# Kernel tuning notes

Measured on AMD Instinct MI355X. Metric: run time of the kernel, lower is better.

## Reference

```python
import jax, jax.numpy as jnp
import numpy as np


def _multinomial_sample(t, gumbel, k):
    # t: [R, S] non-negative weights (R = batch*hidden). Torch's
    # torch.multinomial(t, k) (without replacement) is distributionally
    # equivalent to top-k of log(t) + Gumbel noise (Gumbel top-k trick).
    row_sum = jnp.sum(t, axis=1, keepdims=True)          # [R, 1]
    mask = (row_sum == 0).astype(t.dtype)                # [R, 1]
    t = t + mask                                         # zero rows -> uniform
    scores = jnp.log(t) + gumbel                         # log(0) = -inf: never picked
    _, idx = jax.lax.top_k(scores, k)                    # [R, k] sampled w/o replacement
    vals = jnp.take_along_axis(t, idx, axis=1)           # gather sampled weights
    vals = vals + mask * (-1.0)                          # undo the +1 on masked rows
    return vals.sum(axis=1)                              # [R]


def setup_inputs() -> dict:
    key = jax.random.key(0)
    k1, k2, k3, k4 = jax.random.split(key, 4)
    B, S, H = 8, 4096, 1024
    hidden_states = jax.random.normal(k1, (B, S, H), dtype=jnp.float32)
    u = jax.random.uniform(k2, (B * H, S), dtype=jnp.float32, minval=1e-6, maxval=1.0)
    gumbel = -jnp.log(-jnp.log(u))
    W = jax.random.normal(k3, (H, H), dtype=jnp.float32) * 0.02
    b = jax.random.normal(k4, (H,), dtype=jnp.float32) * 0.02
    return {"hidden_states": hidden_states, "gumbel": gumbel, "W": W, "b": b, "sample": 8}


def reference(hidden_states, gumbel, W, b, sample):
    B, S, H = hidden_states.shape
    rep = jax.nn.relu(hidden_states)                     # [B, S, H]
    t = rep.transpose(0, 2, 1).reshape(-1, S)            # [B*H, S]
    pooled = _multinomial_sample(t, gumbel, sample).reshape(B, H)
    out = pooled @ W.T + b                               # nn.Linear(H, H)
    return jnp.tanh(out)
```

## Files before the change

kernel.cpp:

```cpp
#include <hip/hip_runtime.h>
#include <math.h>

#define BB 8
#define SS 4096
#define HH 1024
#define ROWS (BB * HH)
#define KTOP 8

#define INSERT8(TS, TV, SCV, VALV) do {                                   \
    if ((SCV) > TS[7]) {                                                  \
      TS[7] = (SCV); TV[7] = (VALV);                                      \
      _Pragma("unroll")                                                   \
      for (int _i = 7; _i > 0; --_i) {                                    \
        if (TS[_i] > TS[_i - 1]) {                                        \
          float _t = TS[_i]; TS[_i] = TS[_i - 1]; TS[_i - 1] = _t;        \
          float _v = TV[_i]; TV[_i] = TV[_i - 1]; TV[_i - 1] = _v;        \
        }                                                                 \
      }                                                                   \
    }                                                                     \
  } while (0)

__global__ __launch_bounds__(256) void topk_partial(
    const float* __restrict__ hidden, const float* __restrict__ gumbel,
    float2* __restrict__ pairs, int SC) {
  const int tid = threadIdx.x;
  const int sc  = blockIdx.x;
  const int rb  = blockIdx.y;
  const int r   = rb * 256 + tid;
  const int b   = rb >> 2;
  const int h0  = (rb & 3) << 8;
  const int s0  = sc * SC;

  const float* __restrict__ hcol = hidden + (size_t)b * SS * HH + h0 + tid;
  const float* __restrict__ grow = gumbel + (size_t)r * SS;

  float ts[KTOP], tv[KTOP];
#pragma unroll
  for (int i = 0; i < KTOP; ++i) { ts[i] = -INFINITY; tv[i] = 0.0f; }

  for (int ss = 0; ss < SC; ss += 8) {
    const int s = s0 + ss;
    const float4 g0 = *(const float4*)&grow[s];
    const float4 g1 = *(const float4*)&grow[s + 4];
    const float* __restrict__ hp = hcol + (size_t)s * HH;
    float h[8];
#pragma unroll
    for (int i = 0; i < 8; ++i) h[i] = hp[(size_t)i * HH];
    const float g[8] = {g0.x, g0.y, g0.z, g0.w, g1.x, g1.y, g1.z, g1.w};
#pragma unroll
    for (int i = 0; i < 8; ++i) {
      const float t   = fmaxf(h[i], 0.0f);
      const float scv = logf(t) + g[i];
      INSERT8(ts, tv, scv, t);
    }
  }
#pragma unroll
  for (int j = 0; j < KTOP; ++j)
    pairs[(size_t)(sc * KTOP + j) * ROWS + r] = make_float2(ts[j], tv[j]);
}

__global__ __launch_bounds__(256) void topk_merge(
    const float2* __restrict__ pairs, float* __restrict__ pooled, int NS) {
  __shared__ float2 ls[64 * 4 * KTOP];
  const int tid  = threadIdx.x;
  const int rloc = tid >> 2;
  const int q    = tid & 3;
  const int r    = blockIdx.x * 64 + rloc;

  float ts[KTOP], tv[KTOP];
#pragma unroll
  for (int i = 0; i < KTOP; ++i) { ts[i] = -INFINITY; tv[i] = 0.0f; }

  const int per = (NS + 3) >> 2;
  const int c0  = q * per;
  const int c1  = (c0 + per < NS) ? (c0 + per) : NS;
  for (int c = c0; c < c1; ++c) {
#pragma unroll
    for (int j = 0; j < KTOP; ++j) {
      const float2 p = pairs[(size_t)(c * KTOP + j) * ROWS + r];
      INSERT8(ts, tv, p.x, p.y);
    }
  }
#pragma unroll
  for (int j = 0; j < KTOP; ++j)
    ls[(rloc * 4 + q) * KTOP + j] = make_float2(ts[j], tv[j]);
  __syncthreads();
  if (q == 0) {
    for (int qq = 1; qq < 4; ++qq) {
#pragma unroll
      for (int j = 0; j < KTOP; ++j) {
        const float2 p = ls[(rloc * 4 + qq) * KTOP + j];
        INSERT8(ts, tv, p.x, p.y);
      }
    }
    float sum = 0.0f;
#pragma unroll
    for (int j = 0; j < KTOP; ++j) sum += tv[j];
    pooled[r] = sum;
  }
}

__global__ __launch_bounds__(256) void linear_tanh(
    const float* __restrict__ pooled, const float* __restrict__ W,
    const float* __restrict__ bias, float* __restrict__ out) {
  __shared__ float lp[ROWS];
  const int tid = threadIdx.x;
#pragma unroll
  for (int i = 0; i < ROWS / 4 / 256; ++i)
    ((float4*)lp)[i * 256 + tid] = ((const float4*)pooled)[i * 256 + tid];
  __syncthreads();

  const int wave = tid >> 6;
  const int lane = tid & 63;
  const int j = blockIdx.x * 4 + wave;

  float acc[BB];
#pragma unroll
  for (int bb = 0; bb < BB; ++bb) acc[bb] = 0.0f;
#pragma unroll
  for (int k0 = 0; k0 < HH; k0 += 256) {
    const float4 w4 = *(const float4*)&W[(size_t)j * HH + k0 + lane * 4];
#pragma unroll
    for (int bb = 0; bb < BB; ++bb) {
      const float4 p4 = *(const float4*)&lp[bb * HH + k0 + lane * 4];
      acc[bb] += w4.x * p4.x + w4.y * p4.y + w4.z * p4.z + w4.w * p4.w;
    }
  }
#pragma unroll
  for (int bb = 0; bb < BB; ++bb) {
    float a = acc[bb];
    for (int off = 32; off > 0; off >>= 1) a += __shfl_down(a, off, 64);
    if (lane == 0) out[(size_t)bb * HH + j] = tanhf(a + bias[j]);
  }
}

extern "C" void kernel_launch(void* const* d_in, const int* in_sizes, int n_in,
                              void* d_out, int out_size, void* d_ws, size_t ws_size,
                              hipStream_t stream) {
  const float* hidden = (const float*)d_in[0];
  const float* gumbel = (const float*)d_in[1];
  const float* W      = (const float*)d_in[2];
  const float* bias   = (const float*)d_in[3];
  float* out          = (float*)d_out;

  int NS = 32;
  while (NS > 1) {
    const size_t need = (size_t)NS * KTOP * ROWS * sizeof(float2)
                        + (size_t)ROWS * sizeof(float);
    if (need <= ws_size) break;
    NS >>= 1;
  }
  float2* pairs = (float2*)d_ws;
  float*  pooled = (float*)((char*)d_ws
                   + (size_t)NS * KTOP * ROWS * sizeof(float2));
  const int SC = SS / NS;

  topk_partial<<<dim3(NS, 32), dim3(256), 0, stream>>>(hidden, gumbel, pairs, SC);
  topk_merge<<<dim3(ROWS / 64), dim3(256), 0, stream>>>(pairs, pooled, NS);
  linear_tanh<<<dim3(HH / 4), dim3(256), 0, stream>>>(pooled, W, bias, out);
}
```

Measured before the change: 339.7 us.

## Split each partial top-k chunk across four waves and reduce in shared memory

```diff
diff --git a/kernel.cpp b/kernel.cpp
--- a/kernel.cpp
+++ b/kernel.cpp
@@ -6,6 +6,10 @@
 #define HH 1024
 #define ROWS (BB * HH)
 #define KTOP 8
+#define NS 32
+#define SC (SS / NS)
+#define SCW (SC / 4)
+#define NB (SCW / 8)
 
 #define INSERT8(TS, TV, SCV, VALV) do {                                   \
     if ((SCV) > TS[7]) {                                                  \
@@ -22,76 +26,136 @@
 
 __global__ __launch_bounds__(256) void topk_partial(
     const float* __restrict__ hidden, const float* __restrict__ gumbel,
-    float2* __restrict__ pairs, int SC) {
+    float2* __restrict__ pairs) {
+  __shared__ float2 lst[256 * 9];
+
   const int tid = threadIdx.x;
+  const int rl  = tid & 63;
+  const int w   = tid >> 6;
   const int sc  = blockIdx.x;
   const int rb  = blockIdx.y;
-  const int r   = rb * 256 + tid;
-  const int b   = rb >> 2;
-  const int h0  = (rb & 3) << 8;
-  const int s0  = sc * SC;
-
-  const float* __restrict__ hcol = hidden + (size_t)b * SS * HH + h0 + tid;
-  const float* __restrict__ grow = gumbel + (size_t)r * SS;
+  const int r   = rb * 64 + rl;
+  const int b   = rb >> 4;
+  const int h0  = (rb & 15) << 6;
+  const int s_base = sc * SC + w * SCW;
+
+  const float* __restrict__ hcol = hidden + ((size_t)b * SS) * HH + h0 + rl;
+  const float4* __restrict__ gp =
+      (const float4*)(gumbel + (size_t)r * SS + s_base);
 
   float ts[KTOP], tv[KTOP];
 #pragma unroll
   for (int i = 0; i < KTOP; ++i) { ts[i] = -INFINITY; tv[i] = 0.0f; }
 
-  for (int ss = 0; ss < SC; ss += 8) {
-    const int s = s0 + ss;
-    const float4 g0 = *(const float4*)&grow[s];
-    const float4 g1 = *(const float4*)&grow[s + 4];
-    const float* __restrict__ hp = hcol + (size_t)s * HH;
-    float h[8];
-#pragma unroll
-    for (int i = 0; i < 8; ++i) h[i] = hp[(size_t)i * HH];
-    const float g[8] = {g0.x, g0.y, g0.z, g0.w, g1.x, g1.y, g1.z, g1.w};
+  float4 ga = gp[0], gb = gp[1];
+  float hb[8];
+  {
+    const float* __restrict__ hp = hcol + (size_t)s_base * HH;
+#pragma unroll
+    for (int i = 0; i < 8; ++i) hb[i] = hp[(size_t)i * HH];
+  }
+#pragma unroll
+  for (int k = 0; k < NB; ++k) {
+    float4 gna, gnb; float hn[8];
+    if (k + 1 < NB) {
+      gna = gp[2 * k + 2]; gnb = gp[2 * k + 3];
+      const float* __restrict__ hp = hcol + (size_t)(s_base + 8 * (k + 1)) * HH;
+#pragma unroll
+      for (int i = 0; i < 8; ++i) hn[i] = hp[(size_t)i * HH];
+    }
+    const float g[8] = {ga.x, ga.y, ga.z, ga.w, gb.x, gb.y, gb.z, gb.w};
 #pragma unroll
     for (int i = 0; i < 8; ++i) {
-      const float t   = fmaxf(h[i], 0.0f);
+      const float t   = fmaxf(hb[i], 0.0f);
       const float scv = logf(t) + g[i];
       INSERT8(ts, tv, scv, t);
     }
-  }
+    if (k + 1 < NB) {
+      ga = gna; gb = gnb;
+#pragma unroll
+      for (int i = 0; i < 8; ++i) hb[i] = hn[i];
+    }
+  }
+
 #pragma unroll
   for (int j = 0; j < KTOP; ++j)
-    pairs[(size_t)(sc * KTOP + j) * ROWS + r] = make_float2(ts[j], tv[j]);
+    lst[(w * 64 + rl) * 9 + j] = make_float2(ts[j], tv[j]);
+  __syncthreads();
+  if (w == 0 || w == 2) {
+#pragma unroll
+    for (int j = 0; j < KTOP; ++j) {
+      const float2 p = lst[((w + 1) * 64 + rl) * 9 + j];
+      INSERT8(ts, tv, p.x, p.y);
+    }
+    if (w == 2) {
+#pragma unroll
+      for (int j = 0; j < KTOP; ++j)
+        lst[(2 * 64 + rl) * 9 + j] = make_float2(ts[j], tv[j]);
+    }
+  }
+  __syncthreads();
+  if (w == 0) {
+#pragma unroll
+    for (int j = 0; j < KTOP; ++j) {
+      const float2 p = lst[(2 * 64 + rl) * 9 + j];
+      INSERT8(ts, tv, p.x, p.y);
+    }
+    float2* __restrict__ op = pairs + ((size_t)r * NS + sc) * KTOP;
+#pragma unroll
+    for (int j = 0; j < KTOP; ++j) op[j] = make_float2(ts[j], tv[j]);
+  }
 }
 
 __global__ __launch_bounds__(256) void topk_merge(
-    const float2* __restrict__ pairs, float* __restrict__ pooled, int NS) {
-  __shared__ float2 ls[64 * 4 * KTOP];
+    const float2* __restrict__ pairs, float* __restrict__ pooled) {
+  __shared__ float2 ls[256 * 9];
   const int tid  = threadIdx.x;
-  const int rloc = tid >> 2;
-  const int q    = tid & 3;
-  const int r    = blockIdx.x * 64 + rloc;
+  const int rloc = tid >> 3;
+  const int q    = tid & 7;
+  const int r    = blockIdx.x * 32 + rloc;
+  const int slot = rloc * 8 + q;
 
   float ts[KTOP], tv[KTOP];
 #pragma unroll
   for (int i = 0; i < KTOP; ++i) { ts[i] = -INFINITY; tv[i] = 0.0f; }
 
-  const int per = (NS + 3) >> 2;
-  const int c0  = q * per;
-  const int c1  = (c0 + per < NS) ? (c0 + per) : NS;
-  for (int c = c0; c < c1; ++c) {
-#pragma unroll
-    for (int j = 0; j < KTOP; ++j) {
-      const float2 p = pairs[(size_t)(c * KTOP + j) * ROWS + r];
-      INSERT8(ts, tv, p.x, p.y);
-    }
-  }
-#pragma unroll
-  for (int j = 0; j < KTOP; ++j)
-    ls[(rloc * 4 + q) * KTOP + j] = make_float2(ts[j], tv[j]);
+  const int cpg = NS / 8;
+  const float4* __restrict__ p =
+      (const float4*)(pairs + ((size_t)r * NS + q * cpg) * KTOP);
+#pragma unroll
+  for (int i = 0; i < cpg * KTOP / 2; ++i) {
+    const float4 two = p[i];
+    INSERT8(ts, tv, two.x, two.y);
+    INSERT8(ts, tv, two.z, two.w);
+  }
+#pragma unroll
+  for (int j = 0; j < KTOP; ++j) ls[slot * 9 + j] = make_float2(ts[j], tv[j]);
+  __syncthreads();
+  if ((q & 1) == 0) {
+#pragma unroll
+    for (int j = 0; j < KTOP; ++j) {
+      const float2 pp = ls[(slot + 1) * 9 + j];
+      INSERT8(ts, tv, pp.x, pp.y);
+    }
+#pragma unroll
+    for (int j = 0; j < KTOP; ++j) ls[slot * 9 + j] = make_float2(ts[j], tv[j]);
+  }
+  __syncthreads();
+  if ((q & 3) == 0) {
+#pragma unroll
+    for (int j = 0; j < KTOP; ++j) {
+      const float2 pp = ls[(slot + 2) * 9 + j];
+      INSERT8(ts, tv, pp.x, pp.y);
+    }
+#pragma unroll
+    for (int j = 0; j < KTOP; ++j) ls[slot * 9 + j] = make_float2(ts[j], tv[j]);
+  }
   __syncthreads();
   if (q == 0) {
-    for (int qq = 1; qq < 4; ++qq) {
-#pragma unroll
-      for (int j = 0; j < KTOP; ++j) {
-        const float2 p = ls[(rloc * 4 + qq) * KTOP + j];
-        INSERT8(ts, tv, p.x, p.y);
-      }
+#pragma unroll
+    for (int j = 0; j < KTOP; ++j) {
+      const float2 pp = ls[(slot + 4) * 9 + j];
+      INSERT8(ts, tv, pp.x, pp.y);
     }
     float sum = 0.0f;
 #pragma unroll
@@ -143,19 +207,11 @@
   const float* bias   = (const float*)d_in[3];
   float* out          = (float*)d_out;
 
-  int NS = 32;
-  while (NS > 1) {
-    const size_t need = (size_t)NS * KTOP * ROWS * sizeof(float2)
-                        + (size_t)ROWS * sizeof(float);
-    if (need <= ws_size) break;
-    NS >>= 1;
-  }
-  float2* pairs = (float2*)d_ws;
+  float2* pairs  = (float2*)d_ws;
   float*  pooled = (float*)((char*)d_ws
-                   + (size_t)NS * KTOP * ROWS * sizeof(float2));
-  const int SC = SS / NS;
-
-  topk_partial<<<dim3(NS, 32), dim3(256), 0, stream>>>(hidden, gumbel, pairs, SC);
-  topk_merge<<<dim3(ROWS / 64), dim3(256), 0, stream>>>(pairs, pooled, NS);
+                   + (size_t)ROWS * NS * KTOP * sizeof(float2));
+
+  topk_partial<<<dim3(NS, ROWS / 64), dim3(256), 0, stream>>>(hidden, gumbel, pairs);
+  topk_merge<<<dim3(ROWS / 32), dim3(256), 0, stream>>>(pairs, pooled);
   linear_tanh<<<dim3(HH / 4), dim3(256), 0, stream>>>(pooled, W, bias, out);
 }
```

After: 321.1 us. -5.5%, faster.
